# Optimization experiments

Hardware: AMD Instinct MI355X
Metric: run time of the kernel (lower is better)

The kernel has to match this reference:

```python
import jax, jax.numpy as jnp
import numpy as np

INPUT_DIM = 512
PROJ_DIM = 128
HIDDEN = INPUT_DIM // 2  # 256


def setup_inputs() -> dict:
    key = jax.random.key(0)
    ks = jax.random.split(key, 6)
    B = 8192
    s1 = 1.0 / np.sqrt(INPUT_DIM)
    s2 = 1.0 / np.sqrt(HIDDEN)
    return {
        "fused_text": jax.random.normal(ks[0], (B, INPUT_DIM), dtype=jnp.float32),
        "x": jax.random.normal(ks[1], (B, INPUT_DIM), dtype=jnp.float32),
        # generator layer 1: Linear(input_dim, input_dim//2), torch layout [out, in]
        "W1": jax.random.uniform(ks[2], (HIDDEN, INPUT_DIM), jnp.float32, -s1, s1),
        "b1": jax.random.uniform(ks[3], (HIDDEN,), jnp.float32, -s1, s1),
        # generator layer 2: Linear(input_dim//2, proj_dim * input_dim)
        "W2": jax.random.uniform(ks[4], (PROJ_DIM * INPUT_DIM, HIDDEN), jnp.float32, -s2, s2),
        "b2": jax.random.uniform(ks[5], (PROJ_DIM * INPUT_DIM,), jnp.float32, -s2, s2),
    }


def reference(fused_text, x, W1, b1, W2, b2):
    B = fused_text.shape[0]
    # hypernetwork generator MLP
    h = jax.nn.relu(fused_text @ W1.T + b1)          # [B, hidden]
    w_flat = h @ W2.T + b2                           # [B, proj_dim * input_dim]
    W = w_flat.reshape(B, PROJ_DIM, INPUT_DIM)       # per-sample weights
    # per-sample projection: bmm(W, x[..., None]).squeeze(-1)
    out = jnp.einsum("bpi,bi->bp", W, x)             # [B, proj_dim]
    return out
```

## Files before the change

### kernel.cpp

```cpp
#include <hip/hip_runtime.h>
#include <stdint.h>

#define B_SZ   8192
#define IN_DIM 512
#define HID    256
#define PROJ   128

typedef __attribute__((ext_vector_type(8))) short bf16x8;
typedef __attribute__((ext_vector_type(4))) float f32x4;

#define GLDS16(gp, lp) __builtin_amdgcn_global_load_lds( \
    (const __attribute__((address_space(1))) void*)(gp), \
    (__attribute__((address_space(3))) void*)(lp), 16, 0, 0)

__device__ __forceinline__ unsigned short f2bf(float f) {
    union { float f; uint32_t u; } c; c.f = f;
    uint32_t u = c.u;
    uint32_t r = (u + 0x7fffu + ((u >> 16) & 1u)) >> 16;
    return (unsigned short)r;
}
__device__ __forceinline__ float bfhi(uint32_t v) {
    union { uint32_t u; float f; } c; c.u = v & 0xffff0000u; return c.f;
}
__device__ __forceinline__ float bflo(uint32_t v) {
    union { uint32_t u; float f; } c; c.u = v << 16; return c.f;
}

__global__ __launch_bounds__(256) void k0_prep(
        const float4* __restrict__ W2, ushort4* __restrict__ W2b,
        const float* __restrict__ x, unsigned short* __restrict__ xTb) {
    __shared__ float tile[64][65];
    const int bid = blockIdx.x;
    if (bid < 2048) {
        const int nW2 = (PROJ * IN_DIM * HID) / 4;
        const int stride = 2048 * 256;
        for (int i = bid * 256 + threadIdx.x; i < nW2; i += stride) {
            float4 v = W2[i];
            ushort4 o;
            o.x = f2bf(v.x); o.y = f2bf(v.y); o.z = f2bf(v.z); o.w = f2bf(v.w);
            W2b[i] = o;
        }
    } else {
        const int tb = bid - 2048;
        const int bi = tb & 7, bb = tb >> 3;
        const int i0 = bi * 64, b0 = bb * 64;
        const int t = threadIdx.x;
        const int c = t & 63, r4 = t >> 6;
        #pragma unroll
        for (int rr = 0; rr < 64; rr += 4)
            tile[rr + r4][c] = x[(size_t)(b0 + rr + r4) * IN_DIM + i0 + c];
        __syncthreads();
        #pragma unroll
        for (int rr = 0; rr < 64; rr += 4)
            xTb[(size_t)(i0 + rr + r4) * B_SZ + b0 + c] = f2bf(tile[c][rr + r4]);
    }
}

__device__ __forceinline__ bf16x8 ld_cvt8(const float* __restrict__ s) {
    float4 a = *(const float4*)s;
    float4 b = *(const float4*)(s + 4);
    bf16x8 r;
    r[0] = (short)f2bf(a.x); r[1] = (short)f2bf(a.y);
    r[2] = (short)f2bf(a.z); r[3] = (short)f2bf(a.w);
    r[4] = (short)f2bf(b.x); r[5] = (short)f2bf(b.y);
    r[6] = (short)f2bf(b.z); r[7] = (short)f2bf(b.w);
    return r;
}

__global__ __launch_bounds__(256) void k1_hidden(
        const float* __restrict__ ft,
        const float* __restrict__ W1,
        const float* __restrict__ b1,
        unsigned short* __restrict__ hb) {
    const int lane = threadIdx.x & 63;
    const int wv   = threadIdx.x >> 6;
    const int l15  = lane & 15, q = lane >> 4;
    const int b0 = blockIdx.x * 32;
    const int n0 = wv * 64;

    f32x4 acc[2][4];
    const f32x4 z4 = {0.f, 0.f, 0.f, 0.f};
    #pragma unroll
    for (int mt = 0; mt < 2; ++mt)
        #pragma unroll
        for (int nt = 0; nt < 4; ++nt) acc[mt][nt] = z4;

    for (int kq = 0; kq < 16; ++kq) {
        const int koff = kq * 32 + q * 8;
        bf16x8 a[2], bb[4];
        #pragma unroll
        for (int mt = 0; mt < 2; ++mt)
            a[mt] = ld_cvt8(ft + (size_t)(b0 + mt*16 + l15) * IN_DIM + koff);
        #pragma unroll
        for (int nt = 0; nt < 4; ++nt)
            bb[nt] = ld_cvt8(W1 + (size_t)(n0 + nt*16 + l15) * IN_DIM + koff);
        #pragma unroll
        for (int mt = 0; mt < 2; ++mt)
            #pragma unroll
            for (int nt = 0; nt < 4; ++nt)
                acc[mt][nt] = __builtin_amdgcn_mfma_f32_16x16x32_bf16(
                    a[mt], bb[nt], acc[mt][nt], 0, 0, 0);
    }
    #pragma unroll
    for (int nt = 0; nt < 4; ++nt) {
        float bias = b1[n0 + nt*16 + l15];
        #pragma unroll
        for (int mt = 0; mt < 2; ++mt)
            #pragma unroll
            for (int r = 0; r < 4; ++r) {
                float v = acc[mt][nt][r] + bias;
                v = fmaxf(v, 0.f);
                hb[(size_t)(b0 + mt*16 + q*4 + r) * HID + n0 + nt*16 + l15] = f2bf(v);
            }
    }
}

__global__ __launch_bounds__(256) void k2_bias(
        const float* __restrict__ x,
        const float* __restrict__ b2,
        float* __restrict__ out) {
    const int lane = threadIdx.x & 63;
    const int wv   = threadIdx.x >> 6;
    const int l15  = lane & 15, q = lane >> 4;
    const int b0 = blockIdx.x * 32;
    const int n0 = wv * 32;

    f32x4 acc[2][2];
    const f32x4 z4 = {0.f, 0.f, 0.f, 0.f};
    #pragma unroll
    for (int mt = 0; mt < 2; ++mt)
        #pragma unroll
        for (int nt = 0; nt < 2; ++nt) acc[mt][nt] = z4;

    for (int kq = 0; kq < 16; ++kq) {
        const int koff = kq * 32 + q * 8;
        bf16x8 a[2], bb[2];
        #pragma unroll
        for (int mt = 0; mt < 2; ++mt)
            a[mt] = ld_cvt8(x + (size_t)(b0 + mt*16 + l15) * IN_DIM + koff);
        #pragma unroll
        for (int nt = 0; nt < 2; ++nt)
            bb[nt] = ld_cvt8(b2 + (size_t)(n0 + nt*16 + l15) * IN_DIM + koff);
        #pragma unroll
        for (int mt = 0; mt < 2; ++mt)
            #pragma unroll
            for (int nt = 0; nt < 2; ++nt)
                acc[mt][nt] = __builtin_amdgcn_mfma_f32_16x16x32_bf16(
                    a[mt], bb[nt], acc[mt][nt], 0, 0, 0);
    }
    #pragma unroll
    for (int mt = 0; mt < 2; ++mt)
        #pragma unroll
        for (int nt = 0; nt < 2; ++nt)
            #pragma unroll
            for (int r = 0; r < 4; ++r)
                out[(size_t)(b0 + mt*16 + q*4 + r) * PROJ + n0 + nt*16 + l15]
                    = acc[mt][nt][r];
}

__global__ __launch_bounds__(256, 3) void k3_main(
        const unsigned short* __restrict__ W2b,
        const unsigned short* __restrict__ hb,
        const unsigned short* __restrict__ xTb,
        float* __restrict__ out) {
    __shared__ unsigned short w2t[2][2][32 * 64];
    __shared__ unsigned short xt[32 * 256];
    const int tid  = threadIdx.x;
    const int lane = tid & 63;
    const int wv   = tid >> 6;
    const int l15  = lane & 15, q = lane >> 4;
    const int pgrp = blockIdx.x & 127;
    const int bsup = blockIdx.x >> 7;
    const int p0   = pgrp;
    const int b0blk = bsup * 256;
    const int b0w  = b0blk + wv * 64;
    const f32x4 z4 = {0.f, 0.f, 0.f, 0.f};

    bf16x8 afr[4][4];
    #pragma unroll
    for (int mt = 0; mt < 4; ++mt) {
        const unsigned short* hrow = hb + (size_t)(b0w + mt*16 + l15) * HID + q * 8;
        #pragma unroll
        for (int kq = 0; kq < 4; ++kq)
            afr[mt][kq] = *(const bf16x8*)(hrow + kq * 32);
    }

    const unsigned short* wsp[2];
    #pragma unroll
    for (int jj = 0; jj < 2; ++jj) {
        const int rl = wv*8 + (lane >> 3);
        const int c  = (lane & 7) ^ (lane >> 3);
        wsp[jj] = W2b + ((size_t)p0 * IN_DIM + rl) * HID + jj * 64 + c * 8;
    }
    const unsigned short* xsp[4];
    #pragma unroll
    for (int jj = 0; jj < 4; ++jj) {
        const int r = wv*8 + jj*2 + (lane >> 5);
        const int c = (lane & 31) ^ (r & 7);
        xsp[jj] = xTb + (size_t)r * B_SZ + b0blk + c * 8;
    }

    float oacc[4][4];
    #pragma unroll
    for (int mt = 0; mt < 4; ++mt)
        #pragma unroll
        for (int r = 0; r < 4; ++r) oacc[mt][r] = 0.f;

#define STAGE_W2(BUFI, TT) do {                                           \
    const int _kh = (TT) >> 4, _ic = (TT) & 15;                           \
    const size_t _add = (size_t)(_ic * 32) * HID + _kh * 128;             \
    _Pragma("unroll")                                                     \
    for (int _jj = 0; _jj < 2; ++_jj)                                     \
        GLDS16(wsp[_jj] + _add, &w2t[BUFI][_jj][wv * 512]);               \
} while (0)

#define STAGE_X(TT) do {                                                  \
    const size_t _add = (size_t)(((TT) & 15) * 32) * B_SZ;                \
    _Pragma("unroll")                                                     \
    for (int _jj = 0; _jj < 4; ++_jj)                                     \
        GLDS16(xsp[_jj] + _add, &xt[(wv*8 + _jj*2) * 256]);               \
} while (0)

#define COMPUTE() do {                                                    \
    _Pragma("unroll")                                                     \
    for (int sub = 0; sub < 2; ++sub) {                                   \
        const int rloc = sub*16 + l15;                                    \
        const int sw   = rloc & 7;                                        \
        uint2 xv[4];                                                      \
        _Pragma("unroll")                                                 \
        for (int mt = 0; mt < 4; ++mt) {                                  \
            const int cc = wv*8 + mt*2 + (q >> 1);                        \
            const int ss = cc ^ sw;                                       \
            xv[mt] = *(const uint2*)(&xt[rloc*256 + ss*8 + (q & 1)*4]);   \
        }                                                                 \
        bf16x8 bfr[4];                                                    \
        _Pragma("unroll")                                                 \
        for (int kq = 0; kq < 4; ++kq) {                                  \
            const int khf = kq >> 1;                                      \
            const int ch  = (q + 4*(kq & 1)) ^ sw;                        \
            bfr[kq] = *(const bf16x8*)(Lw + khf*2048 + rloc*64 + ch*8);   \
        }                                                                 \
        f32x4 D[4];                                                       \
        _Pragma("unroll")                                                 \
        for (int mt = 0; mt < 4; ++mt)                                    \
            D[mt] = __builtin_amdgcn_mfma_f32_16x16x32_bf16(              \
                afr[mt][0], bfr[0], z4, 0, 0, 0);                         \
        _Pragma("unroll")                                                 \
        for (int kq = 1; kq < 4; ++kq)                                    \
            _Pragma("unroll")                                             \
            for (int mt = 0; mt < 4; ++mt)                                \
                D[mt] = __builtin_amdgcn_mfma_f32_16x16x32_bf16(          \
                    afr[mt][kq], bfr[kq], D[mt], 0, 0, 0);                \
        _Pragma("unroll")                                                 \
        for (int mt = 0; mt < 4; ++mt) {                                  \
            oacc[mt][0] = fmaf(D[mt][0], bflo(xv[mt].x), oacc[mt][0]);    \
            oacc[mt][1] = fmaf(D[mt][1], bfhi(xv[mt].x), oacc[mt][1]);    \
            oacc[mt][2] = fmaf(D[mt][2], bflo(xv[mt].y), oacc[mt][2]);    \
            oacc[mt][3] = fmaf(D[mt][3], bfhi(xv[mt].y), oacc[mt][3]);    \
        }                                                                 \
    }                                                                     \
} while (0)

    STAGE_W2(0, 0);
    STAGE_X(0);
    STAGE_W2(1, 1);

    #pragma unroll 1
    for (int t = 0; t < 32; ++t) {
        if (t < 31) asm volatile("s_waitcnt vmcnt(2)" ::: "memory");
        else        asm volatile("s_waitcnt vmcnt(0)" ::: "memory");
        __builtin_amdgcn_s_barrier();
        asm volatile("" ::: "memory");

        const unsigned short* Lw = &w2t[t & 1][0][0];
        COMPUTE();

        asm volatile("" ::: "memory");
        __builtin_amdgcn_s_barrier();
        asm volatile("" ::: "memory");

        if (t == 15) {
            #pragma unroll
            for (int mt = 0; mt < 4; ++mt) {
                const unsigned short* hrow =
                    hb + (size_t)(b0w + mt*16 + l15) * HID + 128 + q * 8;
                #pragma unroll
                for (int kq = 0; kq < 4; ++kq)
                    afr[mt][kq] = *(const bf16x8*)(hrow + kq * 32);
            }
        }
        if (t < 31) STAGE_X(t + 1);
        if (t < 30) STAGE_W2(t & 1, t + 2);
    }
#undef STAGE_W2
#undef STAGE_X
#undef COMPUTE

    #pragma unroll
    for (int mt = 0; mt < 4; ++mt)
        #pragma unroll
        for (int r = 0; r < 4; ++r) {
            float v = oacc[mt][r];
            v += __shfl_xor(v, 1, 16);
            v += __shfl_xor(v, 2, 16);
            v += __shfl_xor(v, 4, 16);
            v += __shfl_xor(v, 8, 16);
            if (l15 == 0)
                out[(size_t)(b0w + mt*16 + q*4 + r) * PROJ + p0] += v;
        }
}

extern "C" void kernel_launch(void* const* d_in, const int* in_sizes, int n_in,
                              void* d_out, int out_size, void* d_ws, size_t ws_size,
                              hipStream_t stream) {
    const float* ft = (const float*)d_in[0];
    const float* x  = (const float*)d_in[1];
    const float* W1 = (const float*)d_in[2];
    const float* b1 = (const float*)d_in[3];
    const float* W2 = (const float*)d_in[4];
    const float* b2 = (const float*)d_in[5];
    float* out = (float*)d_out;

    char* ws = (char*)d_ws;
    unsigned short* W2b = (unsigned short*)(ws);
    unsigned short* hb  = (unsigned short*)(ws + 33554432);
    unsigned short* xTb = (unsigned short*)(ws + 37748736);

    hipLaunchKernelGGL(k0_prep, dim3(3072), dim3(256), 0, stream,
        (const float4*)W2, (ushort4*)W2b, x, xTb);
    hipLaunchKernelGGL(k1_hidden, dim3(256), dim3(256), 0, stream, ft, W1, b1, hb);
    hipLaunchKernelGGL(k2_bias, dim3(256), dim3(256), 0, stream, x, b2, out);
    hipLaunchKernelGGL(k3_main, dim3(4096), dim3(256), 0, stream, W2b, hb, xTb, out);
}
```

Measured before the change: 455.3 us.

## Load x tile directly into double-buffered registers and triple-buffer W2 in LDS

Drops the LDS staging of the transposed x tile. Each lane now loads the x values it needs straight from global memory into two alternating register buffers, issued two iterations ahead. The W2 LDS staging goes from double to triple buffering, which removes the second barrier in each loop iteration and lets the next W2 stage be issued before compute. The vmcnt waits are retuned to fit the new number of outstanding loads. In exchange, the x global accesses are narrower and strided across rows, and the extra register buffers add pressure under the occupancy bound.

```diff
diff --git a/kernel.cpp b/kernel.cpp
--- a/kernel.cpp
+++ b/kernel.cpp
@@ -163,8 +163,7 @@
         const unsigned short* __restrict__ hb,
         const unsigned short* __restrict__ xTb,
         float* __restrict__ out) {
-    __shared__ unsigned short w2t[2][2][32 * 64];
-    __shared__ unsigned short xt[32 * 256];
+    __shared__ unsigned short w2t[3][2][32 * 64];
     const int tid  = threadIdx.x;
     const int lane = tid & 63;
     const int wv   = tid >> 6;
@@ -192,19 +191,16 @@
         const int c  = (lane & 7) ^ (lane >> 3);
         wsp[jj] = W2b + ((size_t)p0 * IN_DIM + rl) * HID + jj * 64 + c * 8;
     }
-    const unsigned short* xsp[4];
-    #pragma unroll
-    for (int jj = 0; jj < 4; ++jj) {
-        const int r = wv*8 + jj*2 + (lane >> 5);
-        const int c = (lane & 31) ^ (r & 7);
-        xsp[jj] = xTb + (size_t)r * B_SZ + b0blk + c * 8;
-    }
+
+    const unsigned short* xbase = xTb + (size_t)l15 * B_SZ + b0blk + wv*64 + q*4;
 
     float oacc[4][4];
     #pragma unroll
     for (int mt = 0; mt < 4; ++mt)
         #pragma unroll
         for (int r = 0; r < 4; ++r) oacc[mt][r] = 0.f;
+
+    uint2 xrA[2][4], xrB[2][4];
 
 #define STAGE_W2(BUFI, TT) do {                                           \
     const int _kh = (TT) >> 4, _ic = (TT) & 15;                           \
@@ -214,25 +210,21 @@
         GLDS16(wsp[_jj] + _add, &w2t[BUFI][_jj][wv * 512]);               \
 } while (0)
 
-#define STAGE_X(TT) do {                                                  \
-    const size_t _add = (size_t)(((TT) & 15) * 32) * B_SZ;                \
+#define LOAD_XR(XR, TT) do {                                              \
+    const size_t _ro = (size_t)(((TT) & 15) * 32) * B_SZ;                 \
     _Pragma("unroll")                                                     \
-    for (int _jj = 0; _jj < 4; ++_jj)                                     \
-        GLDS16(xsp[_jj] + _add, &xt[(wv*8 + _jj*2) * 256]);               \
+    for (int _s = 0; _s < 2; ++_s)                                        \
+        _Pragma("unroll")                                                 \
+        for (int _mt = 0; _mt < 4; ++_mt)                                 \
+            XR[_s][_mt] = *(const uint2*)(xbase + _ro                     \
+                + (size_t)(_s * 16) * B_SZ + _mt * 16);                   \
 } while (0)
 
-#define COMPUTE() do {                                                    \
+#define COMPUTE(XR) do {                                                  \
     _Pragma("unroll")                                                     \
     for (int sub = 0; sub < 2; ++sub) {                                   \
         const int rloc = sub*16 + l15;                                    \
         const int sw   = rloc & 7;                                        \
-        uint2 xv[4];                                                      \
-        _Pragma("unroll")                                                 \
-        for (int mt = 0; mt < 4; ++mt) {                                  \
-            const int cc = wv*8 + mt*2 + (q >> 1);                        \
-            const int ss = cc ^ sw;                                       \
-            xv[mt] = *(const uint2*)(&xt[rloc*256 + ss*8 + (q & 1)*4]);   \
-        }                                                                 \
         bf16x8 bfr[4];                                                    \
         _Pragma("unroll")                                                 \
         for (int kq = 0; kq < 4; ++kq) {                                  \
@@ -253,31 +245,31 @@
                     afr[mt][kq], bfr[kq], D[mt], 0, 0, 0);                \
         _Pragma("unroll")                                                 \
         for (int mt = 0; mt < 4; ++mt) {                                  \
-            oacc[mt][0] = fmaf(D[mt][0], bflo(xv[mt].x), oacc[mt][0]);    \
-            oacc[mt][1] = fmaf(D[mt][1], bfhi(xv[mt].x), oacc[mt][1]);    \
-            oacc[mt][2] = fmaf(D[mt][2], bflo(xv[mt].y), oacc[mt][2]);    \
-            oacc[mt][3] = fmaf(D[mt][3], bfhi(xv[mt].y), oacc[mt][3]);    \
+            oacc[mt][0] = fmaf(D[mt][0], bflo(XR[sub][mt].x), oacc[mt][0]); \
+            oacc[mt][1] = fmaf(D[mt][1], bfhi(XR[sub][mt].x), oacc[mt][1]); \
+            oacc[mt][2] = fmaf(D[mt][2], bflo(XR[sub][mt].y), oacc[mt][2]); \
+            oacc[mt][3] = fmaf(D[mt][3], bfhi(XR[sub][mt].y), oacc[mt][3]); \
         }                                                                 \
     }                                                                     \
 } while (0)
 
     STAGE_W2(0, 0);
-    STAGE_X(0);
+    LOAD_XR(xrA, 0);
     STAGE_W2(1, 1);
+    LOAD_XR(xrB, 1);
 
     #pragma unroll 1
     for (int t = 0; t < 32; ++t) {
-        if (t < 31) asm volatile("s_waitcnt vmcnt(2)" ::: "memory");
-        else        asm volatile("s_waitcnt vmcnt(0)" ::: "memory");
+        if (t == 16)     asm volatile("s_waitcnt vmcnt(8)"  ::: "memory");
+        else if (t < 31) asm volatile("s_waitcnt vmcnt(10)" ::: "memory");
+        else             asm volatile("s_waitcnt vmcnt(0)"  ::: "memory");
         __builtin_amdgcn_s_barrier();
         asm volatile("" ::: "memory");
 
-        const unsigned short* Lw = &w2t[t & 1][0][0];
-        COMPUTE();
-
-        asm volatile("" ::: "memory");
-        __builtin_amdgcn_s_barrier();
-        asm volatile("" ::: "memory");
+        if (t < 30) STAGE_W2((t + 2) % 3, t + 2);
+
+        const unsigned short* Lw = &w2t[t % 3][0][0];
+        if (t & 1) COMPUTE(xrB); else COMPUTE(xrA);
 
         if (t == 15) {
             #pragma unroll
@@ -289,11 +281,13 @@
                     afr[mt][kq] = *(const bf16x8*)(hrow + kq * 32);
             }
         }
-        if (t < 31) STAGE_X(t + 1);
-        if (t < 30) STAGE_W2(t & 1, t + 2);
+        if (t < 30) {
+            if (t & 1) LOAD_XR(xrB, t + 2);
+            else       LOAD_XR(xrA, t + 2);
+        }
     }
 #undef STAGE_W2
-#undef STAGE_X
+#undef LOAD_XR
 #undef COMPUTE
 
     #pragma unroll
```

After: 1.085 ms. 138% more time.
